# Performance work log

Measured on AMD Instinct MI355X. Metric: run time of the kernel, lower is better.

## Reference

```python
import jax, jax.numpy as jnp
import numpy as np

N_NODES = 100000
IN_CH = 256
H1, C1 = 8, 8   # conv1: heads=8, out_channels=8
H2, C2 = 1, 3   # conv2: heads=1, out_channels=3
NEG_SLOPE = 0.2
EPS = 1e-16


def gat_conv(x, src, dst, W, a_src, a_dst, b, heads, out_ch, n_nodes):
    """PyG-style GATConv (eval mode, self-loops already in src/dst)."""
    h = (x @ W).reshape(n_nodes, heads, out_ch)          # [N,H,C]
    alpha_s = jnp.einsum('nhc,hc->nh', h, a_src)         # [N,H]
    alpha_d = jnp.einsum('nhc,hc->nh', h, a_dst)         # [N,H]
    e = alpha_s[src] + alpha_d[dst]                      # [E,H]
    e = jnp.where(e > 0, e, NEG_SLOPE * e)               # leaky_relu(0.2)
    # segment softmax over destination nodes
    m = jax.ops.segment_max(e, dst, num_segments=n_nodes)
    m = jnp.where(jnp.isfinite(m), m, 0.0)
    ex = jnp.exp(e - m[dst])
    s = jax.ops.segment_sum(ex, dst, num_segments=n_nodes)
    a = ex / (s[dst] + EPS)                              # [E,H]
    msg = h[src] * a[:, :, None]                         # [E,H,C]
    out = jax.ops.segment_sum(msg, dst, num_segments=n_nodes)  # [N,H,C]
    return out.reshape(n_nodes, heads * out_ch) + b


def setup_inputs() -> dict:
    key = jax.random.key(0)
    ks = jax.random.split(key, 10)
    x = jax.random.normal(ks[0], (N_NODES, IN_CH), dtype=jnp.float32)
    edge_index = jax.random.randint(ks[1], (2, 3200000), 0, N_NODES, dtype=jnp.int64)
    sc = 0.1
    return {
        'x': x,
        'edge_index': edge_index,
        'W1': jax.random.normal(ks[2], (IN_CH, H1 * C1), dtype=jnp.float32) * sc,
        'a_src1': jax.random.normal(ks[3], (H1, C1), dtype=jnp.float32) * sc,
        'a_dst1': jax.random.normal(ks[4], (H1, C1), dtype=jnp.float32) * sc,
        'b1': jnp.zeros((H1 * C1,), dtype=jnp.float32),
        'W2': jax.random.normal(ks[5], (H1 * C1, H2 * C2), dtype=jnp.float32) * sc,
        'a_src2': jax.random.normal(ks[6], (H2, C2), dtype=jnp.float32) * sc,
        'a_dst2': jax.random.normal(ks[7], (H2, C2), dtype=jnp.float32) * sc,
        'b2': jnp.zeros((H2 * C2,), dtype=jnp.float32),
    }


def reference(x, edge_index, W1, a_src1, a_dst1, b1, W2, a_src2, a_dst2, b2):
    n = x.shape[0]
    loop = jnp.arange(n, dtype=edge_index.dtype)
    src = jnp.concatenate([edge_index[0], loop])  # add_self_loops=True
    dst = jnp.concatenate([edge_index[1], loop])
    h = gat_conv(x, src, dst, W1, a_src1, a_dst1, b1, H1, C1, n)
    h = jax.nn.elu(h)
    out = gat_conv(h, src, dst, W2, a_src2, a_dst2, b2, H2, C2, n)
    return out
```

## Files before the change

### kernel.cpp

```cpp
#include <hip/hip_runtime.h>
#include <hip/hip_bf16.h>

#define P_W1  0
#define P_AS1 16384
#define P_AD1 16448
#define P_B1  16512
#define P_W2  16576
#define P_AS2 16768
#define P_AD2 16771
#define P_B2  16774

#define NBLK_CSR 512
#define G1GRID   1024

typedef __attribute__((ext_vector_type(8))) short short8;
typedef __attribute__((ext_vector_type(8))) unsigned short ushort8v;
typedef __attribute__((ext_vector_type(4))) float floatx4;

__device__ __forceinline__ float ldf(const void* p, int i, int bf) {
  if (bf) {
    unsigned v = ((unsigned)((const unsigned short*)p)[i]) << 16;
    float f; __builtin_memcpy(&f, &v, 4); return f;
  }
  return ((const float*)p)[i];
}
__device__ __forceinline__ int ldi(const void* p, long i, int i64) {
  return i64 ? ((const int*)p)[2*i] : ((const int*)p)[i];
}
__device__ __forceinline__ unsigned short f2bfbits(float f) {
  __hip_bfloat16 b = __float2bfloat16(f);
  unsigned short u; __builtin_memcpy(&u, &b, 2); return u;
}
__device__ __forceinline__ float bf2f(unsigned short u) {
  unsigned v = ((unsigned)u) << 16;
  float f; __builtin_memcpy(&f, &v, 4); return f;
}

__device__ __forceinline__ void bar_lgkm() {
  __builtin_amdgcn_sched_barrier(0);
  asm volatile("s_waitcnt lgkmcnt(0)" ::: "memory");
  __builtin_amdgcn_s_barrier();
  __builtin_amdgcn_sched_barrier(0);
}

__global__ void k_prep(const void* x, const void* ei,
                       const void* w1, const void* as1, const void* ad1, const void* b1,
                       const void* w2, const void* as2, const void* ad2, const void* b2,
                       int* flags, float* params, unsigned short* w1t) {
  __shared__ int sh[2];
  int tid = threadIdx.x, lane = tid & 63, w = tid >> 6;
  if (w == 0) {
    const unsigned* xw = (const unsigned*)x;
    int hits = 0;
    for (int i = lane; i < 256; i += 64) {
      unsigned b = (xw[i] >> 7) & 0xFF;
      hits += (b >= 96 && b <= 141) ? 1 : 0;
    }
    for (int o = 32; o >= 1; o >>= 1) hits += __shfl_xor(hits, o);
    if (lane == 0) sh[0] = (hits >= 160) ? 1 : 0;
  } else if (w == 1) {
    const unsigned* ew = (const unsigned*)ei;
    int z = 0;
    for (int i = lane; i < 128; i += 64) z += (ew[2*i+1] == 0u) ? 1 : 0;
    for (int o = 32; o >= 1; o >>= 1) z += __shfl_xor(z, o);
    if (lane == 0) sh[1] = (z >= 64) ? 1 : 0;
  }
  __syncthreads();
  int bf = sh[0];
  if (tid == 0) { flags[0] = sh[0]; flags[1] = sh[1]; }
  for (int i = tid; i < 16384; i += blockDim.x) {
    int ch = i >> 8, k = i & 255;
    w1t[i] = f2bfbits(ldf(w1, k * 64 + ch, bf));
  }
  if (!bf) {
    for (int i = tid; i < 16384; i += blockDim.x) params[P_W1 + i] = ldf(w1, i, bf);
  }
  for (int i = tid; i < 64; i += blockDim.x) {
    params[P_AS1 + i] = ldf(as1, i, bf);
    params[P_AD1 + i] = ldf(ad1, i, bf);
    params[P_B1  + i] = ldf(b1,  i, bf);
  }
  for (int i = tid; i < 192; i += blockDim.x) params[P_W2 + i] = ldf(w2, i, bf);
  for (int i = tid; i < 3; i += blockDim.x) {
    params[P_AS2 + i] = ldf(as2, i, bf);
    params[P_AD2 + i] = ldf(ad2, i, bf);
    params[P_B2  + i] = ldf(b2,  i, bf);
  }
}

__global__ void k_bcount(const void* ei, const int* flags, int* gcnt, int* brsv,
                         int E0, int N, int NB, int chunk) {
  __shared__ int h[256];
  int tid = threadIdx.x;
  int i64 = flags[1];
  for (int j = tid; j < NB; j += 256) h[j] = 0;
  __syncthreads();
  int E = E0 + N;
  int b0 = blockIdx.x * chunk, b1 = min(b0 + chunk, E);
  for (int e = b0 + tid; e < b1; e += 256) {
    int dst = (e < E0) ? ldi(ei, (long)E0 + e, i64) : (e - E0);
    atomicAdd(&h[dst >> 9], 1);
  }
  __syncthreads();
  for (int j = tid; j < NB; j += 256)
    brsv[blockIdx.x * NB + j] = atomicAdd(&gcnt[j], h[j]);
}

__global__ void k_bbase(const int* gcnt, int* bbase, int NB) {
  __shared__ int sh[256];
  int tid = threadIdx.x;
  sh[tid] = (tid < NB) ? gcnt[tid] : 0;
  __syncthreads();
  int own = sh[tid];
  for (int ofs = 1; ofs < 256; ofs <<= 1) {
    int v = (tid >= ofs) ? sh[tid - ofs] : 0;
    __syncthreads();
    sh[tid] += v;
    __syncthreads();
  }
  if (tid < NB) bbase[tid] = sh[tid] - own;
  if (tid == NB - 1) bbase[NB] = sh[tid];
}

__global__ void k_bscatter(const void* ei, const int* flags, const int* bbase,
                           const int* brsv, unsigned* pairs, int E0, int N, int NB, int chunk) {
  __shared__ int base_s[256];
  __shared__ int rnk[256];
  int i64 = flags[1], tid = threadIdx.x;
  for (int j = tid; j < NB; j += 256) {
    base_s[j] = bbase[j] + brsv[blockIdx.x * NB + j];
    rnk[j] = 0;
  }
  __syncthreads();
  int E = E0 + N;
  int b0 = blockIdx.x * chunk, b1 = min(b0 + chunk, E);
  for (int e = b0 + tid; e < b1; e += 256) {
    int src, dst;
    if (e < E0) { src = ldi(ei, e, i64); dst = ldi(ei, (long)E0 + e, i64); }
    else        { src = e - E0; dst = src; }
    int bkt = dst >> 9;
    int r = atomicAdd(&rnk[bkt], 1);
    pairs[base_s[bkt] + r] = ((unsigned)src << 9) | (unsigned)(dst & 511);
  }
}

__global__ void k_bsort(const unsigned* pairs, const int* bbase, int* rowp,
                        int* srcs, int N, int NB, int E) {
  __shared__ int h0[512], sc[512], rk[512];
  int b = blockIdx.x, tid = threadIdx.x;
  int s0 = bbase[b], s1 = bbase[b + 1], L = s1 - s0;
  for (int j = tid; j < 512; j += 256) { h0[j] = 0; rk[j] = 0; }
  __syncthreads();
  for (int i = tid; i < L; i += 256) atomicAdd(&h0[pairs[s0 + i] & 511], 1);
  __syncthreads();
  for (int j = tid; j < 512; j += 256) sc[j] = h0[j];
  __syncthreads();
  for (int ofs = 1; ofs < 512; ofs <<= 1) {
    int j0 = tid, j1 = tid + 256;
    int v0 = (j0 >= ofs) ? sc[j0 - ofs] : 0;
    int v1 = (j1 >= ofs) ? sc[j1 - ofs] : 0;
    __syncthreads();
    sc[j0] += v0; sc[j1] += v1;
    __syncthreads();
  }
  for (int j = tid; j < 512; j += 256) {
    int off = sc[j] - h0[j];
    int node = (b << 9) + j;
    if (node < N) rowp[node] = s0 + off;
    sc[j] = off;
  }
  if (b == 0 && tid == 0) rowp[N] = E;
  __syncthreads();
  for (int i = tid; i < L; i += 256) {
    unsigned p = pairs[s0 + i];
    int j = p & 511;
    int r = atomicAdd(&rk[j], 1);
    srcs[s0 + sc[j] + r] = (int)(p >> 9);
  }
}

__device__ __forceinline__ void gemm1_f32(const float* x, const float* params,
                                          unsigned short* h1, float* a_s, float* a_d,
                                          int N, int wave, int lane) {
  int n0 = wave * 4;
  if (n0 >= N) return;
  int nb[4];
#pragma unroll
  for (int j = 0; j < 4; j++) nb[j] = min(n0 + j, N - 1) * 256;
  float acc[4] = {0.f, 0.f, 0.f, 0.f};
  const float* W = params + P_W1;
  for (int k = 0; k < 256; k++) {
    float wv = W[k * 64 + lane];
#pragma unroll
    for (int j = 0; j < 4; j++) acc[j] += x[nb[j] + k] * wv;
  }
  float as1v = params[P_AS1 + lane], ad1v = params[P_AD1 + lane];
#pragma unroll
  for (int j = 0; j < 4; j++) {
    int n = n0 + j;
    if (n >= N) break;
    float hv = acc[j];
    float s = hv * as1v, d = hv * ad1v;
    s += __shfl_xor(s, 1); s += __shfl_xor(s, 2); s += __shfl_xor(s, 4);
    d += __shfl_xor(d, 1); d += __shfl_xor(d, 2); d += __shfl_xor(d, 4);
    h1[(size_t)n * 64 + lane] = f2bfbits(hv);
    if ((lane & 7) == 0) {
      a_s[n * 8 + (lane >> 3)] = s;
      a_d[n * 8 + (lane >> 3)] = d;
    }
  }
}

__global__ void k_gemm1(const void* x, const unsigned short* w1t, const int* flags,
                        const float* params, unsigned short* h1, float* a_s, float* a_d, int N) {
  __shared__ __align__(16) char smem[32768];
  int tid = threadIdx.x;
  int w = tid >> 6, lane = tid & 63;
  if (flags[0]) {
    int NT = (N + 31) >> 5;
    int l16 = lane & 15, quad = lane >> 4;
    int ch = w * 16 + l16;
    const char* xb = (const char*)x;

    auto stage = [&](int t, int bsel) {
      int row0 = t << 5;
      char* buf = smem + bsel * 16384;
#pragma unroll
      for (int jj = 0; jj < 4; jj++) {
        int g = w * 256 + jj * 64 + lane;
        int r = g >> 5;
        int c = g & 31;
        int gr = row0 + r; if (gr >= N) gr = N - 1;
        const char* src = xb + (size_t)gr * 512 + (size_t)((c << 4) ^ ((r & 7) << 4));
        char* dst = buf + g * 16;
        __builtin_amdgcn_global_load_lds((const __attribute__((address_space(1))) unsigned int*)src,
                                         (__attribute__((address_space(3))) unsigned int*)dst,
                                         16, 0, 0);
      }
    };

    short8 bfr[8];
    const unsigned short* wp = w1t + (size_t)ch * 256 + quad * 8;
#pragma unroll
    for (int i = 0; i < 8; i++) bfr[i] = *(const short8*)(wp + i * 32);
    __builtin_amdgcn_sched_barrier(0);

    int t0 = blockIdx.x;
    if (t0 < NT) stage(t0, 0);
    int cur = 0;
    for (int t = t0; t < NT; t += G1GRID) {
      __syncthreads();
      if (t + G1GRID < NT) stage(t + G1GRID, cur ^ 1);
      int row0 = t << 5;
      const char* buf = smem + cur * 16384;
      floatx4 acc[2];
#pragma unroll
      for (int rg = 0; rg < 2; rg++) {
        floatx4 a4 = {0.f, 0.f, 0.f, 0.f};
        int r = rg * 16 + l16;
        const char* arow = buf + r * 512;
        int swz = (r & 7) << 4;
#pragma unroll
        for (int i = 0; i < 8; i++) {
          short8 afr = *(const short8*)(arow + ((quad * 16 + i * 64) ^ swz));
          a4 = __builtin_amdgcn_mfma_f32_16x16x32_bf16(afr, bfr[i], a4, 0, 0, 0);
        }
        acc[rg] = a4;
      }
      bar_lgkm();
      float* ht = (float*)(smem + cur * 16384);
#pragma unroll
      for (int rg = 0; rg < 2; rg++)
#pragma unroll
        for (int rr = 0; rr < 4; rr++)
          ht[(rg * 16 + quad * 4 + rr) * 67 + ch] = acc[rg][rr];
      bar_lgkm();
      int nl = tid >> 3, head = tid & 7;
      int n = row0 + nl;
      if (n < N) {
        const float* hr = ht + nl * 67 + head * 8;
        float s = 0.f, d = 0.f;
        ushort8v u;
#pragma unroll
        for (int c = 0; c < 8; c++) {
          float v = hr[c];
          s += v * params[P_AS1 + head * 8 + c];
          d += v * params[P_AD1 + head * 8 + c];
          u[c] = f2bfbits(v);
        }
        *(ushort8v*)(h1 + (size_t)n * 64 + head * 8) = u;
        a_s[n * 8 + head] = s;
        a_d[n * 8 + head] = d;
      }
      cur ^= 1;
    }
  } else {
    int NW = (N + 3) >> 2;
    for (int task = blockIdx.x * 4 + w; task < NW; task += G1GRID * 4)
      gemm1_f32((const float*)x, params, h1, a_s, a_d, N, task, lane);
  }
}

__global__ void k_agg1(const float* params, const unsigned short* h1, const float* a_s,
                       const float* a_d, const int* rowp, const int* srcs,
                       float4* pk, float* ad2, int N) {
  int n = blockIdx.x * (blockDim.x >> 6) + (threadIdx.x >> 6);
  int lane = threadIdx.x & 63;
  if (n >= N) return;
  int start = rowp[n], end = rowp[n + 1];
  int h = lane & 7, es = lane >> 3;
  float adh = a_d[n * 8 + h];
  float m = -1e30f;
  for (int i = start + es; i < end; i += 8) {
    float e = a_s[srcs[i] * 8 + h] + adh;
    e = e > 0.f ? e : 0.2f * e;
    m = fmaxf(m, e);
  }
  m = fmaxf(m, __shfl_xor(m, 8));
  m = fmaxf(m, __shfl_xor(m, 16));
  m = fmaxf(m, __shfl_xor(m, 32));
  float acc[8] = {0.f,0.f,0.f,0.f,0.f,0.f,0.f,0.f};
  float ssum = 0.f;
  for (int i = start + es; i < end; i += 8) {
    int s = srcs[i];
    float e = a_s[s * 8 + h] + adh;
    e = e > 0.f ? e : 0.2f * e;
    float ex = __expf(e - m);
    ssum += ex;
    ushort8v u = *(const ushort8v*)(h1 + (size_t)s * 64 + h * 8);
#pragma unroll
    for (int c = 0; c < 8; c++) acc[c] += ex * bf2f(u[c]);
  }
#pragma unroll
  for (int msk = 8; msk <= 32; msk <<= 1) {
    ssum += __shfl_xor(ssum, msk);
#pragma unroll
    for (int c = 0; c < 8; c++) acc[c] += __shfl_xor(acc[c], msk);
  }
  if (es == 0) {
    float inv = 1.f / (ssum + 1e-16f);
    float pj0 = 0.f, pj1 = 0.f, pj2 = 0.f;
#pragma unroll
    for (int c = 0; c < 8; c++) {
      float v = acc[c] * inv + params[P_B1 + h * 8 + c];
      v = v > 0.f ? v : (__expf(v) - 1.f);
      const float* w2r = params + P_W2 + (h * 8 + c) * 3;
      pj0 += v * w2r[0]; pj1 += v * w2r[1]; pj2 += v * w2r[2];
    }
    pj0 += __shfl_xor(pj0, 1); pj1 += __shfl_xor(pj1, 1); pj2 += __shfl_xor(pj2, 1);
    pj0 += __shfl_xor(pj0, 2); pj1 += __shfl_xor(pj1, 2); pj2 += __shfl_xor(pj2, 2);
    pj0 += __shfl_xor(pj0, 4); pj1 += __shfl_xor(pj1, 4); pj2 += __shfl_xor(pj2, 4);
    if (h == 0) {
      float as2 = pj0*params[P_AS2+0] + pj1*params[P_AS2+1] + pj2*params[P_AS2+2];
      float ad2v = pj0*params[P_AD2+0] + pj1*params[P_AD2+1] + pj2*params[P_AD2+2];
      pk[n] = make_float4(pj0, pj1, pj2, as2);
      ad2[n] = ad2v;
    }
  }
}

__global__ void k_agg2(const float* params, const float4* pk, const float* ad2,
                       const int* rowp, const int* srcs, void* out, const int* flags, int N) {
  int wid = blockIdx.x * (blockDim.x >> 6) + (threadIdx.x >> 6);
  int lane = threadIdx.x & 63;
  int g = lane >> 4, t = lane & 15;
  int n = wid * 4 + g;
  if (n >= N) return;
  int start = rowp[n], end = rowp[n + 1];
  float ad = ad2[n];
  float m = -1e30f;
  for (int i = start + t; i < end; i += 16) {
    float e = pk[srcs[i]].w + ad;
    e = e > 0.f ? e : 0.2f * e;
    m = fmaxf(m, e);
  }
#pragma unroll
  for (int msk = 1; msk <= 8; msk <<= 1) m = fmaxf(m, __shfl_xor(m, msk));
  float ssum = 0.f, c0 = 0.f, c1 = 0.f, c2 = 0.f;
  for (int i = start + t; i < end; i += 16) {
    float4 v = pk[srcs[i]];
    float e = v.w + ad;
    e = e > 0.f ? e : 0.2f * e;
    float ex = __expf(e - m);
    ssum += ex;
    c0 += ex * v.x; c1 += ex * v.y; c2 += ex * v.z;
  }
#pragma unroll
  for (int msk = 1; msk <= 8; msk <<= 1) {
    ssum += __shfl_xor(ssum, msk);
    c0 += __shfl_xor(c0, msk); c1 += __shfl_xor(c1, msk); c2 += __shfl_xor(c2, msk);
  }
  if (t == 0) {
    float inv = 1.f / (ssum + 1e-16f);
    float o0 = c0 * inv + params[P_B2+0];
    float o1 = c1 * inv + params[P_B2+1];
    float o2 = c2 * inv + params[P_B2+2];
    if (flags[0]) {
      __hip_bfloat16* ob = (__hip_bfloat16*)out;
      ob[n*3+0] = __float2bfloat16(o0);
      ob[n*3+1] = __float2bfloat16(o1);
      ob[n*3+2] = __float2bfloat16(o2);
    } else {
      float* of = (float*)out;
      of[n*3+0] = o0; of[n*3+1] = o1; of[n*3+2] = o2;
    }
  }
}

extern "C" void kernel_launch(void* const* d_in, const int* in_sizes, int n_in,
                              void* d_out, int out_size, void* d_ws, size_t ws_size,
                              hipStream_t stream) {
  const void* x  = d_in[0];
  const void* ei = d_in[1];
  int N  = in_sizes[0] / 256;
  int E0 = in_sizes[1] / 2;
  int E  = E0 + N;
  int NB = (N + 511) >> 9;
  int chunk = (E + NBLK_CSR - 1) / NBLK_CSR;

  char* w = (char*)d_ws;
  size_t off = 0;
  auto alloc = [&](size_t bytes) -> char* {
    char* p = w + off;
    off += (bytes + 255) & ~(size_t)255;
    return p;
  };
  int*            flags  = (int*)           alloc(256);
  float*          params = (float*)         alloc(17408 * 4);
  unsigned short* w1t    = (unsigned short*)alloc(16384 * 2);
  unsigned short* h1     = (unsigned short*)alloc((size_t)N * 64 * 2);
  float*          a_s1   = (float*)         alloc((size_t)N * 8 * 4);
  float*          a_d1   = (float*)         alloc((size_t)N * 8 * 4);
  float4*         pk     = (float4*)        alloc((size_t)N * 16);
  float*          ad2    = (float*)         alloc((size_t)N * 4);
  int*            gcnt   = (int*)           alloc(256 * 4);
  int*            bbase  = (int*)           alloc(257 * 4);
  int*            brsv   = (int*)           alloc((size_t)NBLK_CSR * NB * 4);
  int*            rowp   = (int*)           alloc((size_t)(N + 1) * 4);
  unsigned*       pairs  = (unsigned*)      alloc((size_t)E * 4);
  int*            srcs   = (int*)           alloc((size_t)E * 4);
  (void)ws_size; (void)n_in; (void)out_size;

  hipMemsetAsync(gcnt, 0, 256 * 4, stream);
  k_prep<<<1, 256, 0, stream>>>(x, ei, d_in[2], d_in[3], d_in[4], d_in[5],
                                d_in[6], d_in[7], d_in[8], d_in[9], flags, params, w1t);
  k_gemm1<<<dim3(G1GRID), 256, 0, stream>>>(x, w1t, flags, params, h1, a_s1, a_d1, N);
  k_bcount<<<dim3(NBLK_CSR), 256, 0, stream>>>(ei, flags, gcnt, brsv, E0, N, NB, chunk);
  k_bbase<<<1, 256, 0, stream>>>(gcnt, bbase, NB);
  k_bscatter<<<dim3(NBLK_CSR), 256, 0, stream>>>(ei, flags, bbase, brsv, pairs, E0, N, NB, chunk);
  k_bsort<<<dim3(NB), 256, 0, stream>>>(pairs, bbase, rowp, srcs, N, NB, E);
  k_agg1<<<dim3((N + 3) / 4), 256, 0, stream>>>(params, h1, a_s1, a_d1, rowp, srcs, pk, ad2, N);
  k_agg2<<<dim3((N + 15) / 16), 256, 0, stream>>>(params, pk, ad2, rowp, srcs, d_out, flags, N);
}
```

Before: 682.9 us.

## Use online softmax in aggregation kernels and vectorize edge-index loads in CSR build

Both aggregation kernels drop their separate max pass over each node's edges and compute the softmax in one pass with running-max rescaling, combining partial (max, sum, acc) states across lanes with a log-sum-exp style merge. This removes a second gather of srcs and a_s/pk per edge. The CSR bucket count and scatter kernels now process two edges per thread with int2/int4 vector loads, and chunk is rounded to even for alignment. The cost is extra exp calls whenever the running max increases, plus more shuffles and exps in the reduction.

```diff
diff --git a/kernel.cpp b/kernel.cpp
--- a/kernel.cpp
+++ b/kernel.cpp
@@ -97,9 +97,18 @@
   __syncthreads();
   int E = E0 + N;
   int b0 = blockIdx.x * chunk, b1 = min(b0 + chunk, E);
-  for (int e = b0 + tid; e < b1; e += 256) {
-    int dst = (e < E0) ? ldi(ei, (long)E0 + e, i64) : (e - E0);
-    atomicAdd(&h[dst >> 9], 1);
+  const int* ep = (const int*)ei;
+  for (int e = b0 + tid * 2; e < b1; e += 512) {
+    int d0, d1;
+    if (e + 1 < E0) {
+      if (i64) { int4 v = *(const int4*)(ep + 2 * ((long)E0 + e)); d0 = v.x; d1 = v.z; }
+      else     { int2 v = *(const int2*)(ep + (long)E0 + e);       d0 = v.x; d1 = v.y; }
+    } else {
+      d0 = (e < E0)     ? ldi(ei, (long)E0 + e, i64)     : (e - E0);
+      d1 = (e + 1 < E0) ? ldi(ei, (long)E0 + e + 1, i64) : (e + 1 - E0);
+    }
+    atomicAdd(&h[d0 >> 9], 1);
+    if (e + 1 < b1) atomicAdd(&h[d1 >> 9], 1);
   }
   __syncthreads();
   for (int j = tid; j < NB; j += 256)
@@ -134,13 +143,33 @@
   __syncthreads();
   int E = E0 + N;
   int b0 = blockIdx.x * chunk, b1 = min(b0 + chunk, E);
-  for (int e = b0 + tid; e < b1; e += 256) {
-    int src, dst;
-    if (e < E0) { src = ldi(ei, e, i64); dst = ldi(ei, (long)E0 + e, i64); }
-    else        { src = e - E0; dst = src; }
-    int bkt = dst >> 9;
-    int r = atomicAdd(&rnk[bkt], 1);
-    pairs[base_s[bkt] + r] = ((unsigned)src << 9) | (unsigned)(dst & 511);
+  const int* ep = (const int*)ei;
+  for (int e = b0 + tid * 2; e < b1; e += 512) {
+    int s0v, s1v, d0, d1;
+    if (e + 1 < E0) {
+      if (i64) {
+        int4 vs = *(const int4*)(ep + 2 * (long)e);        s0v = vs.x; s1v = vs.z;
+        int4 vd = *(const int4*)(ep + 2 * ((long)E0 + e)); d0 = vd.x;  d1 = vd.z;
+      } else {
+        int2 vs = *(const int2*)(ep + (long)e);            s0v = vs.x; s1v = vs.y;
+        int2 vd = *(const int2*)(ep + (long)E0 + e);       d0 = vd.x;  d1 = vd.y;
+      }
+    } else {
+      if (e < E0) { s0v = ldi(ei, e, i64);     d0 = ldi(ei, (long)E0 + e, i64); }
+      else        { s0v = e - E0;              d0 = s0v; }
+      if (e + 1 < E0) { s1v = ldi(ei, e + 1, i64); d1 = ldi(ei, (long)E0 + e + 1, i64); }
+      else            { s1v = e + 1 - E0;          d1 = s1v; }
+    }
+    {
+      int bkt = d0 >> 9;
+      int r = atomicAdd(&rnk[bkt], 1);
+      pairs[base_s[bkt] + r] = ((unsigned)s0v << 9) | (unsigned)(d0 & 511);
+    }
+    if (e + 1 < b1) {
+      int bkt = d1 >> 9;
+      int r = atomicAdd(&rnk[bkt], 1);
+      pairs[base_s[bkt] + r] = ((unsigned)s1v << 9) | (unsigned)(d1 & 511);
+    }
   }
 }
 
@@ -310,21 +339,19 @@
   int start = rowp[n], end = rowp[n + 1];
   int h = lane & 7, es = lane >> 3;
   float adh = a_d[n * 8 + h];
-  float m = -1e30f;
-  for (int i = start + es; i < end; i += 8) {
-    float e = a_s[srcs[i] * 8 + h] + adh;
-    e = e > 0.f ? e : 0.2f * e;
-    m = fmaxf(m, e);
-  }
-  m = fmaxf(m, __shfl_xor(m, 8));
-  m = fmaxf(m, __shfl_xor(m, 16));
-  m = fmaxf(m, __shfl_xor(m, 32));
+  float m = -1e30f, ssum = 0.f;
   float acc[8] = {0.f,0.f,0.f,0.f,0.f,0.f,0.f,0.f};
-  float ssum = 0.f;
   for (int i = start + es; i < end; i += 8) {
     int s = srcs[i];
     float e = a_s[s * 8 + h] + adh;
     e = e > 0.f ? e : 0.2f * e;
+    if (e > m) {
+      float sc = __expf(m - e);
+      ssum *= sc;
+#pragma unroll
+      for (int c = 0; c < 8; c++) acc[c] *= sc;
+      m = e;
+    }
     float ex = __expf(e - m);
     ssum += ex;
     ushort8v u = *(const ushort8v*)(h1 + (size_t)s * 64 + h * 8);
@@ -333,9 +360,17 @@
   }
 #pragma unroll
   for (int msk = 8; msk <= 32; msk <<= 1) {
-    ssum += __shfl_xor(ssum, msk);
-#pragma unroll
-    for (int c = 0; c < 8; c++) acc[c] += __shfl_xor(acc[c], msk);
+    float mo = __shfl_xor(m, msk);
+    float so = __shfl_xor(ssum, msk);
+    float M = fmaxf(m, mo);
+    float scs = __expf(m - M), sco = __expf(mo - M);
+    ssum = ssum * scs + so * sco;
+#pragma unroll
+    for (int c = 0; c < 8; c++) {
+      float ao = __shfl_xor(acc[c], msk);
+      acc[c] = acc[c] * scs + ao * sco;
+    }
+    m = M;
   }
   if (es == 0) {
     float inv = 1.f / (ssum + 1e-16f);
@@ -368,27 +403,32 @@
   if (n >= N) return;
   int start = rowp[n], end = rowp[n + 1];
   float ad = ad2[n];
-  float m = -1e30f;
-  for (int i = start + t; i < end; i += 16) {
-    float e = pk[srcs[i]].w + ad;
-    e = e > 0.f ? e : 0.2f * e;
-    m = fmaxf(m, e);
-  }
-#pragma unroll
-  for (int msk = 1; msk <= 8; msk <<= 1) m = fmaxf(m, __shfl_xor(m, msk));
-  float ssum = 0.f, c0 = 0.f, c1 = 0.f, c2 = 0.f;
+  float m = -1e30f, ssum = 0.f, c0 = 0.f, c1 = 0.f, c2 = 0.f;
   for (int i = start + t; i < end; i += 16) {
     float4 v = pk[srcs[i]];
     float e = v.w + ad;
     e = e > 0.f ? e : 0.2f * e;
+    if (e > m) {
+      float sc = __expf(m - e);
+      ssum *= sc; c0 *= sc; c1 *= sc; c2 *= sc;
+      m = e;
+    }
     float ex = __expf(e - m);
     ssum += ex;
     c0 += ex * v.x; c1 += ex * v.y; c2 += ex * v.z;
   }
 #pragma unroll
   for (int msk = 1; msk <= 8; msk <<= 1) {
-    ssum += __shfl_xor(ssum, msk);
-    c0 += __shfl_xor(c0, msk); c1 += __shfl_xor(c1, msk); c2 += __shfl_xor(c2, msk);
+    float mo = __shfl_xor(m, msk);
+    float so = __shfl_xor(ssum, msk);
+    float a0 = __shfl_xor(c0, msk), a1 = __shfl_xor(c1, msk), a2 = __shfl_xor(c2, msk);
+    float M = fmaxf(m, mo);
+    float scs = __expf(m - M), sco = __expf(mo - M);
+    ssum = ssum * scs + so * sco;
+    c0 = c0 * scs + a0 * sco;
+    c1 = c1 * scs + a1 * sco;
+    c2 = c2 * scs + a2 * sco;
+    m = M;
   }
   if (t == 0) {
     float inv = 1.f / (ssum + 1e-16f);
@@ -416,7 +456,7 @@
   int E0 = in_sizes[1] / 2;
   int E  = E0 + N;
   int NB = (N + 511) >> 9;
-  int chunk = (E + NBLK_CSR - 1) / NBLK_CSR;
+  int chunk = (((E + NBLK_CSR - 1) / NBLK_CSR) + 1) & ~1;
 
   char* w = (char*)d_ws;
   size_t off = 0;
```

Result: faster. 658.4 us (-3.6%).
